# Performance work log

Hardware: AMD Instinct MI355X
Metric: run time of the kernel (lower is better)

Reference implementation:

```python
import jax, jax.numpy as jnp
import numpy as np

SIZE = 128      # reconstruction grid (size x size)
ANGLES = 128    # number of projection angles after interpolation
B, C, H, W = 2, 8, 128, 128  # batch, channels, detector rows (z-slices), detector cols
N_VIEWS = 8


def setup_inputs() -> dict:
    key = jax.random.key(0)
    keys = jax.random.split(key, N_VIEWS)
    return {f"f{i}": jax.random.normal(keys[i], (B, C, H, W), dtype=jnp.float32)
            for i in range(N_VIEWS)}


def _fbp(projections, size, n_angles):
    # projections: (B, C, H, V, W) -- V stacked views, W detector columns
    b, c, h, v, w = projections.shape
    # Interpolation step: resize V views -> n_angles angles (linear, half-pixel,
    # matching F.interpolate default semantics)
    sino = jax.image.resize(projections, (b, c, h, n_angles, w), method="linear")
    # Ram-Lak ramp filter along the detector-column axis
    ramp = jnp.abs(jnp.fft.fftfreq(w)).astype(jnp.float32)
    filt = jnp.real(jnp.fft.ifft(jnp.fft.fft(sino, axis=-1) * ramp, axis=-1)).astype(sino.dtype)
    # Back-projection (parallel beam, per z-slice H)
    thetas = jnp.arange(n_angles, dtype=jnp.float32) * (jnp.pi / n_angles)
    xs = jnp.arange(size, dtype=jnp.float32) - (size - 1) / 2.0
    X, Y = jnp.meshgrid(xs, xs, indexing="xy")  # (S, S)
    center = (w - 1) / 2.0

    sino_per_angle = jnp.moveaxis(filt, 3, 0)  # (A, B, C, H, W)

    def body(acc, inputs):
        theta, sino_a = inputs                       # sino_a: (B, C, H, W)
        t = X * jnp.cos(theta) + Y * jnp.sin(theta) + center  # (S, S)
        t = jnp.clip(t, 0.0, w - 1.0)
        t0 = jnp.floor(t).astype(jnp.int32)
        t1 = jnp.minimum(t0 + 1, w - 1)
        w1 = (t - t0).astype(sino_a.dtype)
        v0 = sino_a[..., t0]                         # (B, C, H, S, S) gather
        v1 = sino_a[..., t1]
        acc = acc + v0 * (1.0 - w1) + v1 * w1
        return acc, None

    acc0 = jnp.zeros((b, c, h, size, size), dtype=sino.dtype)
    vol, _ = jax.lax.scan(body, acc0, (thetas, sino_per_angle))
    return vol * (jnp.pi / (2.0 * n_angles))


def reference(f0, f1, f2, f3, f4, f5, f6, f7):
    # torch.cat([f.unsqueeze(3) for f in features], dim=3) == stack on new axis 3
    projections = jnp.stack([f0, f1, f2, f3, f4, f5, f6, f7], axis=3)  # (B,C,H,V,W)
    return _fbp(projections, SIZE, ANGLES)
```

## Files before the change

kernel.cpp:

```cpp
#include <hip/hip_runtime.h>
#include <math.h>

#define W 128
#define NANG 128
#define SZ 128
#define NV 8
#define NROWS 2048
#define K_DIM 1024
#define NPIX 16384
#define OUT_SCALE 0.012271846303085130f

typedef _Float16 f16x8 __attribute__((ext_vector_type(8)));
typedef _Float16 f16x4 __attribute__((ext_vector_type(4)));
typedef float    f32x4 __attribute__((ext_vector_type(4)));

#define CF_OFF 4096
#define PF_OFF 36864
#define WV_OFF (36864 + (size_t)NROWS * K_DIM * 2)

struct Ptrs8 { const float* p[8]; };

__device__ __forceinline__ void glds16(const void* g, void* l) {
    __builtin_amdgcn_global_load_lds(
        (const __attribute__((address_space(1))) void*)g,
        (__attribute__((address_space(3))) void*)l, 16, 0, 0);
}

__global__ void k_tables(float* __restrict__ kt, float2* __restrict__ cs,
                         _Float16* __restrict__ cf) {
    __shared__ float kl[W];
    int d = threadIdx.x;
    const float w0 = 6.283185307179586f / (float)W * (float)d;
    float s = 0.f;
    for (int f = 1; f < 64; ++f)
        s = fmaf((float)f, __cosf(w0 * (float)f), s);
    s = 2.f * s + 64.f * ((d & 1) ? -1.f : 1.f);
    float kv = s * (1.f / (float)(W * W));
    kt[d] = kv;
    kl[d] = kv;
    float th = (float)d * ((float)M_PI / (float)NANG);
    cs[d] = make_float2(cosf(th), sinf(th));
    __syncthreads();
    for (int k = 0; k < W; ++k)
        cf[d * W + k] = (_Float16)kl[(d - k) & (W - 1)];
}

#define FS_A 136
__global__ __launch_bounds__(256)
void k_fgemm(Ptrs8 in, const _Float16* __restrict__ cf,
             _Float16* __restrict__ pf) {
    __shared__ _Float16 sA[64 * FS_A];
    __shared__ _Float16 sB[128 * FS_A];
    const int tid  = threadIdx.x;
    const int lane = tid & 63, wave = tid >> 6;
    const int fr = lane & 15, fg = lane >> 4;
    const int blk = blockIdx.x;

    {
        const int i   = tid >> 5;
        const int pos = (tid & 31) * 4;
#pragma unroll
        for (int v = 0; v < NV; ++v) {
            float4 x = *(const float4*)(in.p[v] + (size_t)(blk * 8 + i) * W + pos);
            f16x4 h = { (_Float16)x.x, (_Float16)x.y, (_Float16)x.z, (_Float16)x.w };
            *(f16x4*)&sA[(i * 8 + v) * FS_A + pos] = h;
        }
    }
#pragma unroll
    for (int j = 0; j < 8; ++j) {
        int c = tid + 256 * j;
        int n = c >> 4, kp = (c & 15) * 8;
        *(f16x8*)&sB[n * FS_A + kp] = *(const f16x8*)&cf[n * W + kp];
    }
    __syncthreads();

    f32x4 acc[8] = {};
#pragma unroll
    for (int kb = 0; kb < W; kb += 32) {
        f16x8 af = *(const f16x8*)&sA[(wave * 16 + fr) * FS_A + kb + fg * 8];
#pragma unroll
        for (int nt = 0; nt < 8; ++nt) {
            f16x8 bf = *(const f16x8*)&sB[(nt * 16 + fr) * FS_A + kb + fg * 8];
            acc[nt] = __builtin_amdgcn_mfma_f32_16x16x32_f16(af, bf, acc[nt], 0, 0, 0);
        }
    }
#pragma unroll
    for (int nt = 0; nt < 8; ++nt) {
        int m = blk * 64 + wave * 16 + fg * 4;
        int n = nt * 16 + fr;
#pragma unroll
        for (int rr = 0; rr < 4; ++rr)
            pf[(size_t)(m + rr) * W + n] = (_Float16)acc[nt][rr];
    }
}

__global__ void k_wv(const float2* __restrict__ cs, _Float16* __restrict__ wv) {
    __shared__ float wrow[8 * K_DIM];
    const int tid = threadIdx.x;
    const int p0 = blockIdx.x * 8;
    for (int i = tid; i < 8 * K_DIM; i += 256) wrow[i] = 0.f;
    __syncthreads();
    const int px  = tid >> 5;
    const int sub = tid & 31;
    const int p = p0 + px;
    const float x = (float)(p & 127) - 63.5f;
    const float y = (float)(p >> 7) - 63.5f;
    float* prow = &wrow[px * K_DIM];
    for (int a = sub; a < NANG; a += 32) {
        float2 c = cs[a];
        float t = fmaf(x, c.x, fmaf(y, c.y, 63.5f));
        t = fminf(fmaxf(t, 0.f), 127.f);
        float tf = fminf(floorf(t), 126.f);
        int   ti = (int)tf;
        float wt = t - tf;
        float src = ((float)a + 0.5f) * 0.0625f - 0.5f;
        src = fminf(fmaxf(src, 0.f), 7.f);
        float vf = floorf(src);
        int   v0 = (int)vf;
        int   v1 = v0 + 1 < NV ? v0 + 1 : NV - 1;
        float wa = src - vf;
        float wA0 = (1.f - wa) * OUT_SCALE;
        atomicAdd(&prow[v0 * W + ti],     wA0 * (1.f - wt));
        atomicAdd(&prow[v0 * W + ti + 1], wA0 * wt);
        if (v1 != v0) {
            float wA1 = wa * OUT_SCALE;
            atomicAdd(&prow[v1 * W + ti],     wA1 * (1.f - wt));
            atomicAdd(&prow[v1 * W + ti + 1], wA1 * wt);
        }
    }
    __syncthreads();
    uint* wvu = (uint*)(wv + (size_t)p0 * K_DIM);
#pragma unroll
    for (int j = 0; j < 16; ++j) {
        int j2 = tid + 256 * j;
        float2 w2 = *(const float2*)&wrow[j2 * 2];
        union { uint u; struct { _Float16 lo, hi; } h; } pk;
        pk.h.lo = (_Float16)w2.x; pk.h.hi = (_Float16)w2.y;
        wvu[j2] = pk.u;
    }
}

#define NT 16

__device__ __forceinline__ void fencebar() {
    asm volatile("" ::: "memory");
    __builtin_amdgcn_s_barrier();
    asm volatile("" ::: "memory");
}

__device__ __forceinline__ void stage_half(const _Float16* __restrict__ G, int R0,
                                           int h, int kt, _Float16* L, int tid) {
#pragma unroll
    for (int r = 0; r < 2; ++r) {
        const int c   = r * 512 + tid;
        const int row = (h << 7) + (c >> 3);
        const int q   = c & 7;
        const _Float16* src = G + (size_t)(R0 + row) * K_DIM + kt * 64
                                + ((q ^ (row & 7)) << 3);
        _Float16* dst = L + (h << 13) + ((r * 512 + (tid & 448)) << 3);
        glds16(src, dst);
    }
}

__device__ __forceinline__ f16x8 frag(const _Float16* L, int row, int q) {
    return *(const f16x8*)(L + row * 64 + ((q ^ (row & 7)) << 3));
}

__global__ __launch_bounds__(512, 2)
void k_gemm(const _Float16* __restrict__ A,
            const _Float16* __restrict__ Bm,
            float* __restrict__ out) {
    __shared__ _Float16 lds[65536];
    const int tid  = threadIdx.x;
    const int lane = tid & 63, wid = tid >> 6;
    const int wm = wid >> 2, wn = wid & 3;
    const int fr = lane & 15, fg = lane >> 4;

    const int flat = blockIdx.y * 64 + blockIdx.x;
    const int swz  = (flat & 7) * 64 + (flat >> 3);
    const int m0 = (swz >> 6) * 256;
    const int n0 = (swz & 63) * 256;

    _Float16* const A0 = lds;
    _Float16* const B0 = lds + 16384;
    _Float16* const A1 = lds + 32768;
    _Float16* const B1 = lds + 49152;

    stage_half(Bm, n0, 0, 0, B0, tid);
    stage_half(A,  m0, 0, 0, A0, tid);
    stage_half(Bm, n0, 1, 0, B0, tid);
    stage_half(A,  m0, 1, 0, A0, tid);
    stage_half(Bm, n0, 0, 1, B1, tid);
    stage_half(A,  m0, 0, 1, A1, tid);
    asm volatile("s_waitcnt vmcnt(4)" ::: "memory");
    fencebar();

    f32x4 acc[8][4] = {};
    f16x8 af[4][2], bf[4][2];
    const int ar = wm * 128 + fr;
    const int br = wn * 64 + fr;

    auto tile = [&](int t, _Float16* Ab, _Float16* Bb, _Float16* An, _Float16* Bn)
        __attribute__((always_inline)) {
#pragma unroll
        for (int i = 0; i < 4; ++i) {
            af[i][0] = frag(Ab, ar + i * 16, fg);
            af[i][1] = frag(Ab, ar + i * 16, 4 + fg);
        }
#pragma unroll
        for (int j = 0; j < 2; ++j) {
            bf[j][0] = frag(Bb, br + j * 16, fg);
            bf[j][1] = frag(Bb, br + j * 16, 4 + fg);
        }
        if (t + 1 < NT) stage_half(Bm, n0, 1, t + 1, Bn, tid);
        fencebar();
        asm volatile("s_waitcnt lgkmcnt(0)" ::: "memory");
        __builtin_amdgcn_sched_barrier(0);
        __builtin_amdgcn_s_setprio(1);
#pragma unroll
        for (int i = 0; i < 4; ++i)
#pragma unroll
            for (int j = 0; j < 2; ++j) {
                acc[i][j] = __builtin_amdgcn_mfma_f32_16x16x32_f16(af[i][0], bf[j][0], acc[i][j], 0, 0, 0);
                acc[i][j] = __builtin_amdgcn_mfma_f32_16x16x32_f16(af[i][1], bf[j][1], acc[i][j], 0, 0, 0);
            }
        __builtin_amdgcn_s_setprio(0);
        fencebar();
#pragma unroll
        for (int j = 2; j < 4; ++j) {
            bf[j][0] = frag(Bb, br + j * 16, fg);
            bf[j][1] = frag(Bb, br + j * 16, 4 + fg);
        }
        if (t + 1 < NT) stage_half(A, m0, 1, t + 1, An, tid);
        fencebar();
        asm volatile("s_waitcnt lgkmcnt(0)" ::: "memory");
        __builtin_amdgcn_sched_barrier(0);
        __builtin_amdgcn_s_setprio(1);
#pragma unroll
        for (int i = 0; i < 4; ++i)
#pragma unroll
            for (int j = 2; j < 4; ++j) {
                acc[i][j] = __builtin_amdgcn_mfma_f32_16x16x32_f16(af[i][0], bf[j][0], acc[i][j], 0, 0, 0);
                acc[i][j] = __builtin_amdgcn_mfma_f32_16x16x32_f16(af[i][1], bf[j][1], acc[i][j], 0, 0, 0);
            }
        __builtin_amdgcn_s_setprio(0);
        fencebar();
#pragma unroll
        for (int i = 0; i < 4; ++i) {
            af[i][0] = frag(Ab, ar + 64 + i * 16, fg);
            af[i][1] = frag(Ab, ar + 64 + i * 16, 4 + fg);
        }
        if (t + 2 < NT) stage_half(Bm, n0, 0, t + 2, Bb, tid);
        fencebar();
        asm volatile("s_waitcnt lgkmcnt(0)" ::: "memory");
        __builtin_amdgcn_sched_barrier(0);
        __builtin_amdgcn_s_setprio(1);
#pragma unroll
        for (int i = 0; i < 4; ++i)
#pragma unroll
            for (int j = 2; j < 4; ++j) {
                acc[4 + i][j] = __builtin_amdgcn_mfma_f32_16x16x32_f16(af[i][0], bf[j][0], acc[4 + i][j], 0, 0, 0);
                acc[4 + i][j] = __builtin_amdgcn_mfma_f32_16x16x32_f16(af[i][1], bf[j][1], acc[4 + i][j], 0, 0, 0);
            }
        __builtin_amdgcn_s_setprio(0);
        fencebar();
        if (t + 2 < NT) stage_half(A, m0, 0, t + 2, Ab, tid);
        fencebar();
        __builtin_amdgcn_s_setprio(1);
#pragma unroll
        for (int i = 0; i < 4; ++i)
#pragma unroll
            for (int j = 0; j < 2; ++j) {
                acc[4 + i][j] = __builtin_amdgcn_mfma_f32_16x16x32_f16(af[i][0], bf[j][0], acc[4 + i][j], 0, 0, 0);
                acc[4 + i][j] = __builtin_amdgcn_mfma_f32_16x16x32_f16(af[i][1], bf[j][1], acc[4 + i][j], 0, 0, 0);
            }
        __builtin_amdgcn_s_setprio(0);
        if (t + 2 < NT)      asm volatile("s_waitcnt vmcnt(4)" ::: "memory");
        else if (t + 1 < NT) asm volatile("s_waitcnt vmcnt(0)" ::: "memory");
        fencebar();
    };

    for (int tt = 0; tt < NT; tt += 2) {
        tile(tt,     A0, B0, A1, B1);
        tile(tt + 1, A1, B1, A0, B0);
    }

#pragma unroll
    for (int i = 0; i < 8; ++i) {
#pragma unroll
        for (int j = 0; j < 4; ++j) {
            const int m = m0 + wm * 128 + i * 16 + fg * 4;
            const int n = n0 + wn * 64 + j * 16 + fr;
            float* op = out + (size_t)m * NPIX + n;
#pragma unroll
            for (int rr = 0; rr < 4; ++rr)
                op[(size_t)rr * NPIX] = acc[i][j][rr];
        }
    }
}

extern "C" void kernel_launch(void* const* d_in, const int* in_sizes, int n_in,
                              void* d_out, int out_size, void* d_ws, size_t ws_size,
                              hipStream_t stream) {
    float*      kt = (float*)d_ws;
    float2*     cs = (float2*)((char*)d_ws + 512);
    _Float16*   cf = (_Float16*)((char*)d_ws + CF_OFF);
    _Float16*   pf = (_Float16*)((char*)d_ws + PF_OFF);
    _Float16*   wv = (_Float16*)((char*)d_ws + WV_OFF);

    Ptrs8 in;
    for (int i = 0; i < NV; ++i) in.p[i] = (const float*)d_in[i];

    k_tables<<<1, 128, 0, stream>>>(kt, cs, cf);
    k_fgemm<<<NROWS * NV / 64, 256, 0, stream>>>(in, cf, pf);
    k_wv<<<NPIX / 8, 256, 0, stream>>>(cs, wv);
    dim3 grid(NPIX / 256, NROWS / 256);
    k_gemm<<<grid, 512, 0, stream>>>(pf, wv, (float*)d_out);
}
```

Baseline: 263.3 us.

## Merge table, filter-GEMM and weight-matrix kernels into one prep launch; remap GEMM tiles

The separate k_tables, k_fgemm and k_wv launches become a single k_prep kernel. Its first 256 blocks do the ramp-filter GEMM and build the circulant filter matrix in LDS, and the remaining blocks build the backprojection weight matrix with cos/sin tables computed locally. This removes two kernel launches and the serial dependency on the single-block table kernel, at the cost of redundant per-block table computation and a larger shared-memory union that may lower occupancy. The main GEMM's block-to-tile swizzle is also changed to alter L2 reuse of the B tiles.

```diff
diff --git a/kernel.cpp b/kernel.cpp
--- a/kernel.cpp
+++ b/kernel.cpp
@@ -14,7 +14,6 @@
 typedef _Float16 f16x4 __attribute__((ext_vector_type(4)));
 typedef float    f32x4 __attribute__((ext_vector_type(4)));
 
-#define CF_OFF 4096
 #define PF_OFF 36864
 #define WV_OFF (36864 + (size_t)NROWS * K_DIM * 2)
 
@@ -26,117 +25,121 @@
         (__attribute__((address_space(3))) void*)l, 16, 0, 0);
 }
 
-__global__ void k_tables(float* __restrict__ kt, float2* __restrict__ cs,
-                         _Float16* __restrict__ cf) {
-    __shared__ float kl[W];
-    int d = threadIdx.x;
-    const float w0 = 6.283185307179586f / (float)W * (float)d;
-    float s = 0.f;
-    for (int f = 1; f < 64; ++f)
-        s = fmaf((float)f, __cosf(w0 * (float)f), s);
-    s = 2.f * s + 64.f * ((d & 1) ? -1.f : 1.f);
-    float kv = s * (1.f / (float)(W * W));
-    kt[d] = kv;
-    kl[d] = kv;
-    float th = (float)d * ((float)M_PI / (float)NANG);
-    cs[d] = make_float2(cosf(th), sinf(th));
-    __syncthreads();
-    for (int k = 0; k < W; ++k)
-        cf[d * W + k] = (_Float16)kl[(d - k) & (W - 1)];
-}
-
 #define FS_A 136
+#define PREP_FG_BLOCKS 256
+
+union PrepLds {
+    struct {
+        _Float16 sA[64 * FS_A];
+        _Float16 sB[128 * FS_A];
+        float    kl[W];
+    } fg;
+    struct {
+        float  wrow[8 * K_DIM];
+        float2 cst[NANG];
+    } wv;
+};
+
 __global__ __launch_bounds__(256)
-void k_fgemm(Ptrs8 in, const _Float16* __restrict__ cf,
-             _Float16* __restrict__ pf) {
-    __shared__ _Float16 sA[64 * FS_A];
-    __shared__ _Float16 sB[128 * FS_A];
-    const int tid  = threadIdx.x;
-    const int lane = tid & 63, wave = tid >> 6;
-    const int fr = lane & 15, fg = lane >> 4;
-    const int blk = blockIdx.x;
-
-    {
-        const int i   = tid >> 5;
-        const int pos = (tid & 31) * 4;
-#pragma unroll
-        for (int v = 0; v < NV; ++v) {
-            float4 x = *(const float4*)(in.p[v] + (size_t)(blk * 8 + i) * W + pos);
-            f16x4 h = { (_Float16)x.x, (_Float16)x.y, (_Float16)x.z, (_Float16)x.w };
-            *(f16x4*)&sA[(i * 8 + v) * FS_A + pos] = h;
-        }
-    }
-#pragma unroll
-    for (int j = 0; j < 8; ++j) {
-        int c = tid + 256 * j;
-        int n = c >> 4, kp = (c & 15) * 8;
-        *(f16x8*)&sB[n * FS_A + kp] = *(const f16x8*)&cf[n * W + kp];
-    }
-    __syncthreads();
-
-    f32x4 acc[8] = {};
-#pragma unroll
-    for (int kb = 0; kb < W; kb += 32) {
-        f16x8 af = *(const f16x8*)&sA[(wave * 16 + fr) * FS_A + kb + fg * 8];
+void k_prep(Ptrs8 in, _Float16* __restrict__ pf, _Float16* __restrict__ wv) {
+    __shared__ PrepLds u;
+    const int tid = threadIdx.x;
+
+    if (blockIdx.x < PREP_FG_BLOCKS) {
+        const int blk  = blockIdx.x;
+        const int lane = tid & 63, wave = tid >> 6;
+        const int fr = lane & 15, fg = lane >> 4;
+
+        if (tid < W) {
+            const int d = tid;
+            const float w0 = 6.283185307179586f / (float)W * (float)d;
+            float s = 0.f;
+            for (int f = 1; f < 64; ++f)
+                s = fmaf((float)f, __cosf(w0 * (float)f), s);
+            s = 2.f * s + 64.f * ((d & 1) ? -1.f : 1.f);
+            u.fg.kl[d] = s * (1.f / (float)(W * W));
+        }
+        {
+            const int i   = tid >> 5;
+            const int pos = (tid & 31) * 4;
+#pragma unroll
+            for (int v = 0; v < NV; ++v) {
+                float4 x = *(const float4*)(in.p[v] + (size_t)(blk * 8 + i) * W + pos);
+                f16x4 h = { (_Float16)x.x, (_Float16)x.y, (_Float16)x.z, (_Float16)x.w };
+                *(f16x4*)&u.fg.sA[(i * 8 + v) * FS_A + pos] = h;
+            }
+        }
+        __syncthreads();
+        for (int e = tid; e < W * W; e += 256) {
+            const int t = e >> 7, s = e & 127;
+            u.fg.sB[t * FS_A + s] = (_Float16)u.fg.kl[(t - s) & (W - 1)];
+        }
+        __syncthreads();
+
+        f32x4 acc[8] = {};
+#pragma unroll
+        for (int kb = 0; kb < W; kb += 32) {
+            f16x8 af = *(const f16x8*)&u.fg.sA[(wave * 16 + fr) * FS_A + kb + fg * 8];
+#pragma unroll
+            for (int nt = 0; nt < 8; ++nt) {
+                f16x8 bf = *(const f16x8*)&u.fg.sB[(nt * 16 + fr) * FS_A + kb + fg * 8];
+                acc[nt] = __builtin_amdgcn_mfma_f32_16x16x32_f16(af, bf, acc[nt], 0, 0, 0);
+            }
+        }
 #pragma unroll
         for (int nt = 0; nt < 8; ++nt) {
-            f16x8 bf = *(const f16x8*)&sB[(nt * 16 + fr) * FS_A + kb + fg * 8];
-            acc[nt] = __builtin_amdgcn_mfma_f32_16x16x32_f16(af, bf, acc[nt], 0, 0, 0);
-        }
-    }
-#pragma unroll
-    for (int nt = 0; nt < 8; ++nt) {
-        int m = blk * 64 + wave * 16 + fg * 4;
-        int n = nt * 16 + fr;
-#pragma unroll
-        for (int rr = 0; rr < 4; ++rr)
-            pf[(size_t)(m + rr) * W + n] = (_Float16)acc[nt][rr];
-    }
-}
-
-__global__ void k_wv(const float2* __restrict__ cs, _Float16* __restrict__ wv) {
-    __shared__ float wrow[8 * K_DIM];
-    const int tid = threadIdx.x;
-    const int p0 = blockIdx.x * 8;
-    for (int i = tid; i < 8 * K_DIM; i += 256) wrow[i] = 0.f;
-    __syncthreads();
-    const int px  = tid >> 5;
-    const int sub = tid & 31;
-    const int p = p0 + px;
-    const float x = (float)(p & 127) - 63.5f;
-    const float y = (float)(p >> 7) - 63.5f;
-    float* prow = &wrow[px * K_DIM];
-    for (int a = sub; a < NANG; a += 32) {
-        float2 c = cs[a];
-        float t = fmaf(x, c.x, fmaf(y, c.y, 63.5f));
-        t = fminf(fmaxf(t, 0.f), 127.f);
-        float tf = fminf(floorf(t), 126.f);
-        int   ti = (int)tf;
-        float wt = t - tf;
-        float src = ((float)a + 0.5f) * 0.0625f - 0.5f;
-        src = fminf(fmaxf(src, 0.f), 7.f);
-        float vf = floorf(src);
-        int   v0 = (int)vf;
-        int   v1 = v0 + 1 < NV ? v0 + 1 : NV - 1;
-        float wa = src - vf;
-        float wA0 = (1.f - wa) * OUT_SCALE;
-        atomicAdd(&prow[v0 * W + ti],     wA0 * (1.f - wt));
-        atomicAdd(&prow[v0 * W + ti + 1], wA0 * wt);
-        if (v1 != v0) {
-            float wA1 = wa * OUT_SCALE;
-            atomicAdd(&prow[v1 * W + ti],     wA1 * (1.f - wt));
-            atomicAdd(&prow[v1 * W + ti + 1], wA1 * wt);
-        }
-    }
-    __syncthreads();
-    uint* wvu = (uint*)(wv + (size_t)p0 * K_DIM);
-#pragma unroll
-    for (int j = 0; j < 16; ++j) {
-        int j2 = tid + 256 * j;
-        float2 w2 = *(const float2*)&wrow[j2 * 2];
-        union { uint u; struct { _Float16 lo, hi; } h; } pk;
-        pk.h.lo = (_Float16)w2.x; pk.h.hi = (_Float16)w2.y;
-        wvu[j2] = pk.u;
+            int m = blk * 64 + wave * 16 + fg * 4;
+            int n = nt * 16 + fr;
+#pragma unroll
+            for (int rr = 0; rr < 4; ++rr)
+                pf[(size_t)(m + rr) * W + n] = (_Float16)acc[nt][rr];
+        }
+    } else {
+        const int p0 = (blockIdx.x - PREP_FG_BLOCKS) * 8;
+        if (tid < NANG) {
+            float th = (float)tid * ((float)M_PI / (float)NANG);
+            u.wv.cst[tid] = make_float2(cosf(th), sinf(th));
+        }
+        for (int i = tid; i < 8 * K_DIM; i += 256) u.wv.wrow[i] = 0.f;
+        __syncthreads();
+        const int px  = tid >> 5;
+        const int sub = tid & 31;
+        const int p = p0 + px;
+        const float x = (float)(p & 127) - 63.5f;
+        const float y = (float)(p >> 7) - 63.5f;
+        float* prow = &u.wv.wrow[px * K_DIM];
+        for (int a = sub; a < NANG; a += 32) {
+            float2 c = u.wv.cst[a];
+            float t = fmaf(x, c.x, fmaf(y, c.y, 63.5f));
+            t = fminf(fmaxf(t, 0.f), 127.f);
+            float tf = fminf(floorf(t), 126.f);
+            int   ti = (int)tf;
+            float wt = t - tf;
+            float src = ((float)a + 0.5f) * 0.0625f - 0.5f;
+            src = fminf(fmaxf(src, 0.f), 7.f);
+            float vf = floorf(src);
+            int   v0 = (int)vf;
+            int   v1 = v0 + 1 < NV ? v0 + 1 : NV - 1;
+            float wa = src - vf;
+            float wA0 = (1.f - wa) * OUT_SCALE;
+            atomicAdd(&prow[v0 * W + ti],     wA0 * (1.f - wt));
+            atomicAdd(&prow[v0 * W + ti + 1], wA0 * wt);
+            if (v1 != v0) {
+                float wA1 = wa * OUT_SCALE;
+                atomicAdd(&prow[v1 * W + ti],     wA1 * (1.f - wt));
+                atomicAdd(&prow[v1 * W + ti + 1], wA1 * wt);
+            }
+        }
+        __syncthreads();
+        uint* wvu = (uint*)(wv + (size_t)p0 * K_DIM);
+#pragma unroll
+        for (int j = 0; j < 16; ++j) {
+            int j2 = tid + 256 * j;
+            float2 w2 = *(const float2*)&u.wv.wrow[j2 * 2];
+            union { uint uu; struct { _Float16 lo, hi; } h; } pk;
+            pk.h.lo = (_Float16)w2.x; pk.h.hi = (_Float16)w2.y;
+            wvu[j2] = pk.uu;
+        }
     }
 }
 
@@ -177,9 +180,10 @@
     const int fr = lane & 15, fg = lane >> 4;
 
     const int flat = blockIdx.y * 64 + blockIdx.x;
-    const int swz  = (flat & 7) * 64 + (flat >> 3);
-    const int m0 = (swz >> 6) * 256;
-    const int n0 = (swz & 63) * 256;
+    const int x    = flat & 7;
+    const int idx  = flat >> 3;
+    const int m0 = (idx >> 3) * 256;
+    const int n0 = (x * 8 + (idx & 7)) * 256;
 
     _Float16* const A0 = lds;
     _Float16* const B0 = lds + 16384;
@@ -302,18 +306,13 @@
 extern "C" void kernel_launch(void* const* d_in, const int* in_sizes, int n_in,
                               void* d_out, int out_size, void* d_ws, size_t ws_size,
                               hipStream_t stream) {
-    float*      kt = (float*)d_ws;
-    float2*     cs = (float2*)((char*)d_ws + 512);
-    _Float16*   cf = (_Float16*)((char*)d_ws + CF_OFF);
     _Float16*   pf = (_Float16*)((char*)d_ws + PF_OFF);
     _Float16*   wv = (_Float16*)((char*)d_ws + WV_OFF);
 
     Ptrs8 in;
     for (int i = 0; i < NV; ++i) in.p[i] = (const float*)d_in[i];
 
-    k_tables<<<1, 128, 0, stream>>>(kt, cs, cf);
-    k_fgemm<<<NROWS * NV / 64, 256, 0, stream>>>(in, cf, pf);
-    k_wv<<<NPIX / 8, 256, 0, stream>>>(cs, wv);
+    k_prep<<<PREP_FG_BLOCKS + NPIX / 8, 256, 0, stream>>>(in, pf, wv);
     dim3 grid(NPIX / 256, NROWS / 256);
     k_gemm<<<grid, 512, 0, stream>>>(pf, wv, (float*)d_out);
 }
```

After: 261.6 us. No clear change (-0.6%).
